# Kernel optimization log

Measured on AMD Instinct MI355X. Metric: run time of the kernel, lower is better.

The kernel has to match this reference:

```python
import jax, jax.numpy as jnp
import numpy as np

D_MODEL, D_INNER, D_STATE, D_CONV, NHEADS, HEADDIM, CHUNK = 2048, 4096, 128, 4, 64, 64, 64
CONV_DIM = D_INNER + 2 * D_STATE  # 4352
D_IN_PROJ = 2 * D_INNER + 2 * D_STATE + NHEADS  # 8512
EPS = 1e-5

def setup_inputs() -> dict:
    key = jax.random.key(0)
    ks = jax.random.split(key, 8)
    B, L = 2, 4096
    return {
        'u': jax.random.normal(ks[0], (B, L, D_MODEL), jnp.float32),
        'W_in': jax.random.normal(ks[1], (D_IN_PROJ, D_MODEL), jnp.float32) * 0.02,
        'conv_w': jax.random.normal(ks[2], (CONV_DIM, D_CONV), jnp.float32) * 0.2,
        'conv_b': jax.random.normal(ks[3], (CONV_DIM,), jnp.float32) * 0.02,
        'dt_bias': jax.random.normal(ks[4], (NHEADS,), jnp.float32) * 0.5,
        'A_log': jax.random.normal(ks[5], (NHEADS,), jnp.float32) * 0.5,
        'D': jax.random.normal(ks[6], (NHEADS,), jnp.float32),
        'norm_w': jnp.ones((D_INNER,), jnp.float32),
        'W_out': jax.random.normal(ks[7], (D_MODEL, D_INNER), jnp.float32) * 0.02,
    }

def silu(x):
    return x * jax.nn.sigmoid(x)

def segsum(x):
    # x: (..., T) -> (..., T, T); out[..., i, j] = sum_{j < k <= i} x[..., k], -inf above diag
    T = x.shape[-1]
    xr = jnp.broadcast_to(x[..., None], x.shape + (T,))
    m1 = jnp.tril(jnp.ones((T, T), bool), -1)
    s = jnp.cumsum(jnp.where(m1, xr, 0.0), axis=-2)
    m0 = jnp.tril(jnp.ones((T, T), bool), 0)
    return jnp.where(m0, s, -jnp.inf)

def ssd(x, A, B, C, chunk):
    # x: (b,L,h,p)  A: (b,L,h)  B,C: (b,L,n) shared across heads
    b, L, h, p = x.shape
    c = L // chunk
    x = x.reshape(b, c, chunk, h, p)
    A = A.reshape(b, c, chunk, h).transpose(0, 3, 1, 2)  # b h c l
    B = B.reshape(b, c, chunk, -1)
    C = C.reshape(b, c, chunk, -1)
    A_cs = jnp.cumsum(A, axis=-1)
    Lmat = jnp.exp(segsum(A))  # (b,h,c,l,s)
    Y_diag = jnp.einsum('bcln,bcsn,bhcls,bcshp->bclhp', C, B, Lmat, x)
    decay_states = jnp.exp(A_cs[..., -1:] - A_cs)  # (b,h,c,l)
    states = jnp.einsum('bcln,bhcl,bclhp->bchpn', B, decay_states, x)
    states = jnp.concatenate([jnp.zeros_like(states[:, :1]), states], axis=1)
    A_last = jnp.pad(A_cs[..., -1], ((0, 0), (0, 0), (1, 0)))  # (b,h,c+1)
    decay_chunk = jnp.exp(segsum(A_last))  # (b,h,c+1,c+1)
    new_states = jnp.einsum('bhzc,bchpn->bzhpn', decay_chunk, states)
    states, final = new_states[:, :-1], new_states[:, -1]
    sdo = jnp.exp(A_cs)  # (b,h,c,l)
    Y_off = jnp.einsum('bcln,bchpn,bhcl->bclhp', C, states, sdo)
    return (Y_diag + Y_off).reshape(b, L, h, p), final

def reference(u, W_in, conv_w, conv_b, dt_bias, A_log, D, norm_w, W_out):
    b, L, _ = u.shape
    zxbcdt = jnp.einsum('bld,ed->ble', u, W_in)
    z = zxbcdt[..., :D_INNER]
    xBC = zxbcdt[..., D_INNER:D_INNER + CONV_DIM]
    dt = jax.nn.softplus(zxbcdt[..., -NHEADS:] + dt_bias)  # (b,L,h)
    A = -jnp.exp(A_log)
    da_log = dt * A  # (b,L,h)
    # causal depthwise conv1d (kernel D_CONV, left pad D_CONV-1)
    xp = jnp.pad(xBC, ((0, 0), (D_CONV - 1, 0), (0, 0)))
    xBC = sum(xp[:, k:k + L, :] * conv_w[:, k] for k in range(D_CONV)) + conv_b
    xBC = silu(xBC)
    x = xBC[..., :D_INNER].reshape(b, L, NHEADS, HEADDIM)
    Bm = xBC[..., D_INNER:D_INNER + D_STATE]
    Cm = xBC[..., D_INNER + D_STATE:]
    y, final_state = ssd(x * dt[..., None], da_log, Bm, Cm, CHUNK)
    y = y + x * D[None, None, :, None]
    y = y.reshape(b, L, D_INNER)
    y = y * silu(z)
    y = y * jax.lax.rsqrt(jnp.mean(y * y, axis=-1, keepdims=True) + EPS) * norm_w
    return jnp.einsum('bld,ed->ble', y, W_out)
```

## Files before the change

### kernel.cpp

```cpp
#include <hip/hip_runtime.h>
#include <stdint.h>
#include <stddef.h>

#define SEQ     4096
#define DMODEL  2048
#define DINNER  4096
#define DSTATE  128
#define NH      64
#define HD      64
#define NCHUNK  64
#define CONVDIM 4352
#define DPROJ   8512

typedef __bf16 bf16_t;
typedef __bf16 bf16x8 __attribute__((ext_vector_type(8)));
typedef float  f32x4  __attribute__((ext_vector_type(4)));
typedef unsigned short u16x4 __attribute__((ext_vector_type(4)));

__device__ __forceinline__ void async_cp16(const bf16_t* g, bf16_t* l) {
    __builtin_amdgcn_global_load_lds(
        (const __attribute__((address_space(1))) void*)g,
        (__attribute__((address_space(3))) void*)l,
        16, 0, 0);
}

__global__ __launch_bounds__(256) void zero_out_kernel(float* out, int n) {
    int i = blockIdx.x*256 + threadIdx.x;
    if (i < n) out[i] = 0.f;
}

__global__ void detect_kernel(const unsigned short* norm_w_raw, int* flag) {
    if (threadIdx.x == 0 && blockIdx.x == 0)
        *flag = (norm_w_raw[0] == 0x3F80) ? 1 : 0;
}

__global__ __launch_bounds__(256) void cast_kernel(
    const void* __restrict__ src, size_t elem_off, bf16_t* __restrict__ dst,
    int n, const int* __restrict__ flag)
{
    int i = blockIdx.x*256 + threadIdx.x;
    if (i >= n) return;
    if (*flag) dst[i] = ((const bf16_t*)src)[elem_off + i];
    else       dst[i] = (bf16_t)(((const float*)src)[elem_off + i]);
}

__global__ __launch_bounds__(256) void cast4_kernel(
    const void* __restrict__ src, size_t elem_off, bf16_t* __restrict__ dst,
    int n4, const int* __restrict__ flag)
{
    int i = blockIdx.x*256 + threadIdx.x;
    if (i >= n4) return;
    if (*flag) {
        u16x4 v = *(const u16x4*)((const unsigned short*)src + elem_off + (size_t)i*4);
        *(u16x4*)(dst + (size_t)i*4) = v;
    } else {
        f32x4 v = *(const f32x4*)((const float*)src + elem_off + (size_t)i*4);
        bf16_t o[4];
        #pragma unroll
        for (int j = 0; j < 4; j++) o[j] = (bf16_t)v[j];
        *(u16x4*)(dst + (size_t)i*4) = *(const u16x4*)o;
    }
}

__global__ __launch_bounds__(256) void addp_kernel(
    float* __restrict__ out, const float* __restrict__ part, int n4)
{
    int i = blockIdx.x*256 + threadIdx.x;
    if (i >= n4) return;
    f32x4 a = *(const f32x4*)(out + (size_t)i*4);
    f32x4 b = *(const f32x4*)(part + (size_t)i*4);
    a[0]+=b[0]; a[1]+=b[1]; a[2]+=b[2]; a[3]+=b[3];
    *(f32x4*)(out + (size_t)i*4) = a;
}

__device__ __forceinline__ void stage_half(
    const bf16_t* __restrict__ G, int grow0, int gmaxrow, int gld,
    int kt, bf16_t* lplane, int half, int tid)
{
    #pragma unroll
    for (int q = 0; q < 2; q++) {
        int rloc = half*128 + q*64 + (tid >> 3);
        int grow = grow0 + rloc; if (grow > gmaxrow) grow = gmaxrow;
        int gcol = kt + ((((tid & 7) ^ (rloc & 7))) << 3);
        async_cp16(G + (size_t)grow*gld + gcol, lplane + rloc*64 + ((tid & 7) << 3));
    }
}

#define GMM_READ_A(PLANE, KS)                                                  \
    _Pragma("unroll")                                                          \
    for (int m_ = 0; m_ < 8; m_++) {                                           \
        const int rl_ = wmBase + m_*16 + lrow;                                 \
        afr[m_] = *(const bf16x8*)((PLANE) + rl_*64 + ((((KS)*4+quad) ^ (rl_&7))<<3)); \
    }

#define GMM_READ_B(PLANE, KS, DST)                                             \
    _Pragma("unroll")                                                          \
    for (int n_ = 0; n_ < 4; n_++) {                                           \
        const int rl_ = wnBase + n_*16 + lrow;                                 \
        DST[n_] = *(const bf16x8*)((PLANE) + rl_*64 + ((((KS)*4+quad) ^ (rl_&7))<<3)); \
    }

#define GMM_TAIL(BKARR, NA, NB)                                                \
    __builtin_amdgcn_s_barrier();                                              \
    asm volatile("s_waitcnt lgkmcnt(0)" ::: "memory");                         \
    __builtin_amdgcn_sched_barrier(0);                                         \
    __builtin_amdgcn_s_setprio(1);                                             \
    _Pragma("unroll")                                                          \
    for (int m_ = 0; m_ < 8; m_++) {                                           \
        acc[m_][NA] = __builtin_amdgcn_mfma_f32_16x16x32_bf16(afr[m_], BKARR[NA], acc[m_][NA], 0,0,0); \
        acc[m_][NB] = __builtin_amdgcn_mfma_f32_16x16x32_bf16(afr[m_], BKARR[NB], acc[m_][NB], 0,0,0); \
    }                                                                          \
    __builtin_amdgcn_s_setprio(0);

template <typename OT>
__global__ __launch_bounds__(512, 2) void gemm256_kernel(
    const bf16_t* __restrict__ A, const bf16_t* __restrict__ W,
    OT* C, OT* C2, int M, int N, int K, int lda, int khalf2)
{
    extern __shared__ __align__(16) bf16_t lds[];
    bf16_t* lAa = lds;
    bf16_t* lAb = lds + 16384;
    bf16_t* lBa = lds + 32768;
    bf16_t* lBb = lds + 49152;

    const int tid  = threadIdx.x;
    const int lane = tid & 63;
    const int wid  = tid >> 6;
    const int lrow = lane & 15;
    const int quad = lane >> 4;
    const int wmBase = (wid >> 2) * 128;
    const int wnBase = (wid & 3) * 64;

    int wg = blockIdx.x;
    const int nwg = gridDim.x;
    if ((nwg & 7) == 0) { int cpx = nwg >> 3; wg = (wg & 7)*cpx + (wg >> 3); }

    const int wld = K;
    int kloc = K;
    OT* Cw = C;
    if (khalf2) {
        const int htiles = nwg >> 1;
        kloc = K >> 1;
        if (wg >= htiles) { Cw = C2; wg -= htiles; A += kloc; W += kloc; }
    }

    const int ntx = (N + 255) >> 8;
    const int n0 = (wg % ntx) * 256;
    const int m0 = (wg / ntx) * 256;

    const int NT   = kloc >> 6;
    const int NTm1 = NT - 1;
    const int NT2  = NT >> 1;

    f32x4 acc[8][4] = {};
    bf16x8 afr[8], bk0[4], bk1[4];

    stage_half(A, m0, M-1, lda, 0,  lAa, 0, tid);
    stage_half(A, m0, M-1, lda, 0,  lAa, 1, tid);
    stage_half(W, n0, N-1, wld, 0,  lBa, 0, tid);
    stage_half(W, n0, N-1, wld, 0,  lBa, 1, tid);
    stage_half(A, m0, M-1, lda, 64, lAb, 0, tid);
    asm volatile("s_waitcnt vmcnt(2)" ::: "memory");
    __builtin_amdgcn_s_barrier();

    for (int i = 0; i < NT2; i++) {
        const int ktb = (2*i + 1) * 64;
        const int ktc = ((2*i + 2) & NTm1) * 64;
        const int ktd = ((2*i + 3) & NTm1) * 64;

        GMM_READ_A(lAa, 0)
        GMM_READ_B(lBa, 0, bk0)
        stage_half(A, m0, M-1, lda, ktb, lAb, 1, tid);
        asm volatile("s_waitcnt lgkmcnt(8)" ::: "memory");
        GMM_TAIL(bk0, 0, 1)
        __builtin_amdgcn_s_barrier();
        GMM_READ_B(lBa, 1, bk1)
        stage_half(W, n0, N-1, wld, ktb, lBb, 0, tid);
        GMM_TAIL(bk0, 2, 3)
        __builtin_amdgcn_s_barrier();
        GMM_READ_A(lAa, 1)
        stage_half(W, n0, N-1, wld, ktb, lBb, 1, tid);
        GMM_TAIL(bk1, 0, 1)
        __builtin_amdgcn_s_barrier();
        stage_half(A, m0, M-1, lda, ktc, lAa, 0, tid);
        GMM_TAIL(bk1, 2, 3)
        asm volatile("s_waitcnt vmcnt(2)" ::: "memory");
        __builtin_amdgcn_s_barrier();

        GMM_READ_A(lAb, 0)
        GMM_READ_B(lBb, 0, bk0)
        stage_half(A, m0, M-1, lda, ktc, lAa, 1, tid);
        asm volatile("s_waitcnt lgkmcnt(8)" ::: "memory");
        GMM_TAIL(bk0, 0, 1)
        __builtin_amdgcn_s_barrier();
        GMM_READ_B(lBb, 1, bk1)
        stage_half(W, n0, N-1, wld, ktc, lBa, 0, tid);
        GMM_TAIL(bk0, 2, 3)
        __builtin_amdgcn_s_barrier();
        GMM_READ_A(lAb, 1)
        stage_half(W, n0, N-1, wld, ktc, lBa, 1, tid);
        GMM_TAIL(bk1, 0, 1)
        __builtin_amdgcn_s_barrier();
        stage_half(A, m0, M-1, lda, ktd, lAb, 0, tid);
        GMM_TAIL(bk1, 2, 3)
        asm volatile("s_waitcnt vmcnt(2)" ::: "memory");
        __builtin_amdgcn_s_barrier();
    }

    asm volatile("s_waitcnt vmcnt(0)" ::: "memory");

    #pragma unroll
    for (int m = 0; m < 8; m++) {
        const int row = m0 + wmBase + m*16 + quad*4;
        #pragma unroll
        for (int n = 0; n < 4; n++) {
            const int col = n0 + wnBase + n*16 + lrow;
            if (col < N) {
                #pragma unroll
                for (int rr = 0; rr < 4; rr++)
                    Cw[(size_t)(row + rr)*N + col] = (OT)acc[m][n][rr];
            }
        }
    }
}

__global__ __launch_bounds__(256) void dt_kernel(
    const bf16_t* __restrict__ zx, const bf16_t* __restrict__ dt_bias,
    float* __restrict__ dtb)
{
    int i = blockIdx.x*256 + threadIdx.x;
    int h = i & 63, row = i >> 6;
    float raw = (float)zx[(size_t)row*DPROJ + (DINNER + CONVDIM) + h] + (float)dt_bias[h];
    dtb[i] = (raw > 20.f) ? raw : log1pf(expf(raw));
}

__global__ void cumsum_kernel(
    const float* __restrict__ dtb, const bf16_t* __restrict__ A_log,
    float* __restrict__ Acs)
{
    int blk = blockIdx.x;
    int h = blk & 63, c = blk >> 6;
    int lane = threadIdx.x;
    float Ah = -expf((float)A_log[h]);
    size_t row = (size_t)c*64 + lane;
    float v = dtb[row*64 + h] * Ah;
    #pragma unroll
    for (int off = 1; off < 64; off <<= 1) {
        float t = __shfl_up(v, off, 64);
        if (lane >= off) v += t;
    }
    Acs[(size_t)blk*64 + lane] = v;
}

__global__ __launch_bounds__(256) void conv_kernel(
    const bf16_t* __restrict__ zx, const bf16_t* __restrict__ conv_w,
    const bf16_t* __restrict__ conv_b, bf16_t* __restrict__ xbc)
{
    int i = blockIdx.x*256 + threadIdx.x;
    int cb = i % (CONVDIM/8);
    int l  = i / (CONVDIM/8);
    int ch0 = cb*8;
    const bf16_t* src = zx + (size_t)l*DPROJ + DINNER + ch0;
    float acc[8];
    {
        bf16x8 bv = *(const bf16x8*)(conv_b + ch0);
        #pragma unroll
        for (int j = 0; j < 8; j++) acc[j] = (float)bv[j];
    }
    bf16x8 w4[4];
    #pragma unroll
    for (int t = 0; t < 4; t++) w4[t] = *(const bf16x8*)(conv_w + ch0*4 + t*8);
    #pragma unroll
    for (int k = 0; k < 4; k++) {
        int ll = l - 3 + k;
        if (ll >= 0) {
            bf16x8 v = *(const bf16x8*)(src + (ptrdiff_t)(k-3)*DPROJ);
            #pragma unroll
            for (int j = 0; j < 8; j++)
                acc[j] += (float)v[j] * (float)w4[(j*4+k)>>3][(j*4+k)&7];
        }
    }
    bf16x8 o;
    #pragma unroll
    for (int j = 0; j < 8; j++)
        o[j] = (bf16_t)(acc[j] / (1.f + expf(-acc[j])));
    *(bf16x8*)(xbc + (size_t)i*8) = o;
}

__global__ __launch_bounds__(256) void states_kernel(
    const bf16_t* __restrict__ xbc, const float* __restrict__ dtb,
    const float* __restrict__ Acs, bf16_t* __restrict__ states)
{
    __shared__ __align__(16) bf16_t XsT[64*64];
    __shared__ __align__(16) bf16_t BT[128*64];
    __shared__ float AcsS[64];
    __shared__ float scaleS[64];
    const int blk = blockIdx.x;
    const int h = blk & 63, c = blk >> 6;
    const int tid = threadIdx.x, lane = tid & 63, wid = tid >> 6;
    const size_t rowbase = (size_t)c*64;

    if (tid < 64) AcsS[tid] = Acs[(size_t)blk*64 + tid];
    __syncthreads();
    if (tid < 64) scaleS[tid] = dtb[(rowbase + tid)*64 + h] * expf(AcsS[63] - AcsS[tid]);
    __syncthreads();

    {
        bf16x8 xa[2], b0[2], b1[2];
        #pragma unroll
        for (int half = 0; half < 2; half++) {
            #pragma unroll
            for (int j = 0; j < 8; j++) {
                int l = wid*16 + half*8 + j;
                const bf16_t* rp = xbc + (rowbase + l)*CONVDIM;
                xa[half][j] = (bf16_t)((float)rp[h*64 + lane] * scaleS[l]);
                b0[half][j] = rp[DINNER + lane];
                b1[half][j] = rp[DINNER + 64 + lane];
            }
        }
        #pragma unroll
        for (int half = 0; half < 2; half++) {
            int cch = wid*2 + half;
            *(bf16x8*)(XsT + lane*64       + ((cch ^ (lane & 7))*8)) = xa[half];
            *(bf16x8*)(BT  + lane*64       + ((cch ^ (lane & 7))*8)) = b0[half];
            *(bf16x8*)(BT  + (lane+64)*64  + ((cch ^ (lane & 7))*8)) = b1[half];
        }
    }
    __syncthreads();

    const int lrow = lane & 15, quad = lane >> 4;
    const int waveM = (wid & 1) * 32;
    const int waveN = (wid >> 1) * 64;
    f32x4 acc[2][4] = {};
    #pragma unroll
    for (int ks = 0; ks < 2; ks++) {
        bf16x8 af[2], bfr[4];
        #pragma unroll
        for (int i = 0; i < 2; i++) {
            int p = waveM + i*16 + lrow;
            af[i] = *(const bf16x8*)(XsT + p*64 + (((ks*4 + quad) ^ (p & 7))*8));
        }
        #pragma unroll
        for (int j = 0; j < 4; j++) {
            int n = waveN + j*16 + lrow;
            bfr[j] = *(const bf16x8*)(BT + n*64 + (((ks*4 + quad) ^ (n & 7))*8));
        }
        #pragma unroll
        for (int i = 0; i < 2; i++)
            #pragma unroll
            for (int j = 0; j < 4; j++)
                acc[i][j] = __builtin_amdgcn_mfma_f32_16x16x32_bf16(af[i], bfr[j], acc[i][j], 0, 0, 0);
    }

    const size_t sbase = (size_t)blk*8192;
    #pragma unroll
    for (int i = 0; i < 2; i++)
        #pragma unroll
        for (int j = 0; j < 4; j++) {
            int n = waveN + j*16 + lrow;
            #pragma unroll
            for (int r = 0; r < 4; r++) {
                int p = waveM + i*16 + quad*4 + r;
                states[sbase + (size_t)p*128 + n] = (bf16_t)acc[i][j][r];
            }
        }
}

__global__ __launch_bounds__(256) void gmat_kernel(
    const bf16_t* __restrict__ xbc, float* __restrict__ Gt)
{
    __shared__ __align__(16) float Ct[128*64];
    __shared__ __align__(16) float Bs2[64*128];
    int c = blockIdx.x;
    int tid = threadIdx.x;
    size_t rowbase = (size_t)c*64;
    for (int e = tid; e < 8192; e += 256) {
        int l = e >> 7, n = e & 127;
        const bf16_t* rp = xbc + (rowbase + l)*CONVDIM + DINNER;
        Bs2[e] = (float)rp[n];
        Ct[n*64 + (l ^ (n & 63))] = (float)rp[128 + n];
    }
    __syncthreads();
    int l = tid & 63, s0 = (tid >> 6) * 16;
    float acc[16] = {};
    for (int n4 = 0; n4 < 128; n4 += 4) {
        float c0 = Ct[(n4+0)*64 + (l ^ ((n4+0) & 63))];
        float c1 = Ct[(n4+1)*64 + (l ^ ((n4+1) & 63))];
        float c2 = Ct[(n4+2)*64 + (l ^ ((n4+2) & 63))];
        float c3 = Ct[(n4+3)*64 + (l ^ ((n4+3) & 63))];
        #pragma unroll
        for (int j = 0; j < 16; j++) {
            f32x4 bv = *(const f32x4*)&Bs2[(s0+j)*128 + n4];
            acc[j] += c0*bv[0] + c1*bv[1] + c2*bv[2] + c3*bv[3];
        }
    }
    float* gp = Gt + (size_t)c*4096;
    #pragma unroll
    for (int j = 0; j < 16; j++) gp[l*64 + (s0+j)] = acc[j];
}

__global__ __launch_bounds__(256) void scan_kernel(
    bf16_t* __restrict__ states, const float* __restrict__ Acs)
{
    int i = blockIdx.x*256 + threadIdx.x;
    int n = i & 127, p = (i >> 7) & 63, h = i >> 13;
    size_t off = (size_t)h*8192 + (size_t)p*128 + n;
    const float* ac = Acs + (size_t)h*64 + 63;
    float S = 0.f;
    for (int c = 0; c < 64; c++) {
        float tmp = (float)states[off];
        states[off] = (bf16_t)S;
        S = expf(ac[(size_t)c*4096]) * S + tmp;
        off += (size_t)64*8192;
    }
}

__global__ __launch_bounds__(256) void y_kernel(
    const bf16_t* __restrict__ xbc, const float* __restrict__ dtb,
    const float* __restrict__ Acs, const float* __restrict__ Gt,
    const bf16_t* __restrict__ states, const bf16_t* __restrict__ Dvec,
    bf16_t* __restrict__ y)
{
    __shared__ __align__(16) bf16_t Cs[64*128];
    __shared__ __align__(16) bf16_t Ss[64*128];
    __shared__ __align__(16) bf16_t Wm[64*64];
    __shared__ __align__(16) bf16_t XdT[64*64];
    __shared__ float acsS[64];
    __shared__ float dtS[64];
    const int blk = blockIdx.x;
    const int h = blk & 63, c = blk >> 6;
    const int tid = threadIdx.x, lane = tid & 63, wid = tid >> 6;
    const size_t rowbase = (size_t)c*64;
    const size_t sbase = (size_t)blk*8192;

    if (tid < 64) {
        acsS[tid] = Acs[(size_t)blk*64 + tid];
        dtS[tid]  = dtb[(rowbase + tid)*64 + h];
    }
    __syncthreads();

    #pragma unroll
    for (int it = 0; it < 4; it++) {
        int q = wid*256 + it*64 + lane;
        int l = q >> 4;
        int cl = (q & 15) ^ (l & 7);
        async_cp16(xbc + (rowbase + l)*CONVDIM + DINNER + 128 + cl*8,
                   Cs + (size_t)(wid*256 + it*64)*8);
        async_cp16(states + sbase + (size_t)l*128 + cl*8,
                   Ss + (size_t)(wid*256 + it*64)*8);
    }

    {
        const float* gp = Gt + (size_t)c*4096;
        #pragma unroll
        for (int k = 0; k < 16; k++) {
            int e = k*256 + tid;
            int l = e >> 6, s = e & 63;
            float w = 0.f;
            if (s <= l) w = gp[e] * expf(acsS[l] - acsS[s]);
            Wm[l*64 + (((s >> 3) ^ (l & 7))*8) + (s & 7)] = (bf16_t)w;
        }
    }

    {
        bf16x8 xd[2];
        #pragma unroll
        for (int half = 0; half < 2; half++)
            #pragma unroll
            for (int j = 0; j < 8; j++) {
                int s = wid*16 + half*8 + j;
                xd[half][j] = (bf16_t)((float)xbc[(rowbase + s)*CONVDIM + h*64 + lane] * dtS[s]);
            }
        #pragma unroll
        for (int half = 0; half < 2; half++) {
            int cch = wid*2 + half;
            *(bf16x8*)(XdT + lane*64 + ((cch ^ (lane & 7))*8)) = xd[half];
        }
    }
    __syncthreads();

    const int lrow = lane & 15, quad = lane >> 4;
    const int waveM = (wid & 1) * 32;
    const int waveN = (wid >> 1) * 32;
    f32x4 acc[2][2] = {};

    #pragma unroll
    for (int ks = 0; ks < 4; ks++) {
        bf16x8 af[2], bfr[2];
        #pragma unroll
        for (int i = 0; i < 2; i++) {
            int l = waveM + i*16 + lrow;
            af[i] = *(const bf16x8*)(Cs + l*128 + (((ks*4 + quad) ^ (l & 7))*8));
        }
        #pragma unroll
        for (int j = 0; j < 2; j++) {
            int p = waveN + j*16 + lrow;
            bfr[j] = *(const bf16x8*)(Ss + p*128 + (((ks*4 + quad) ^ (p & 7))*8));
        }
        #pragma unroll
        for (int i = 0; i < 2; i++)
            #pragma unroll
            for (int j = 0; j < 2; j++)
                acc[i][j] = __builtin_amdgcn_mfma_f32_16x16x32_bf16(af[i], bfr[j], acc[i][j], 0, 0, 0);
    }

    #pragma unroll
    for (int i = 0; i < 2; i++)
        #pragma unroll
        for (int r = 0; r < 4; r++) {
            int l = waveM + i*16 + quad*4 + r;
            float el = expf(acsS[l]);
            #pragma unroll
            for (int j = 0; j < 2; j++)
                acc[i][j][r] *= el;
        }

    #pragma unroll
    for (int ks = 0; ks < 2; ks++) {
        bf16x8 af[2], bfr[2];
        #pragma unroll
        for (int i = 0; i < 2; i++) {
            int l = waveM + i*16 + lrow;
            af[i] = *(const bf16x8*)(Wm + l*64 + (((ks*4 + quad) ^ (l & 7))*8));
        }
        #pragma unroll
        for (int j = 0; j < 2; j++) {
            int p = waveN + j*16 + lrow;
            bfr[j] = *(const bf16x8*)(XdT + p*64 + (((ks*4 + quad) ^ (p & 7))*8));
        }
        #pragma unroll
        for (int i = 0; i < 2; i++)
            #pragma unroll
            for (int j = 0; j < 2; j++)
                acc[i][j] = __builtin_amdgcn_mfma_f32_16x16x32_bf16(af[i], bfr[j], acc[i][j], 0, 0, 0);
    }

    const float Dh = (float)Dvec[h];
    #pragma unroll
    for (int i = 0; i < 2; i++)
        #pragma unroll
        for (int r = 0; r < 4; r++) {
            int l = waveM + i*16 + quad*4 + r;
            const bf16_t* xr = xbc + (rowbase + l)*CONVDIM + h*64;
            bf16_t* yr = y + (rowbase + l)*DPROJ + h*64;
            #pragma unroll
            for (int j = 0; j < 2; j++) {
                int p = waveN + j*16 + lrow;
                yr[p] = (bf16_t)(acc[i][j][r] + Dh * (float)xr[p]);
            }
        }
}

__global__ __launch_bounds__(256) void gatenorm_kernel(
    bf16_t* __restrict__ zx, const bf16_t* __restrict__ norm_w)
{
    __shared__ float red[4];
    int row = blockIdx.x;
    int tid = threadIdx.x;
    const bf16_t* zr = zx + (size_t)row*DPROJ;
    bf16_t* yr = zx + (size_t)row*DPROJ + DINNER;
    float vals[16]; float ss = 0.f;
    #pragma unroll
    for (int i = 0; i < 16; i++) {
        int e = i*256 + tid;
        float zv = (float)zr[e];
        float g = (float)yr[e] * (zv / (1.f + expf(-zv)));
        vals[i] = g; ss += g*g;
    }
    #pragma unroll
    for (int off = 32; off >= 1; off >>= 1) ss += __shfl_down(ss, off, 64);
    if ((tid & 63) == 0) red[tid >> 6] = ss;
    __syncthreads();
    float tot = red[0] + red[1] + red[2] + red[3];
    float scale = rsqrtf(tot * (1.f/4096.f) + 1e-5f);
    #pragma unroll
    for (int i = 0; i < 16; i++) {
        int e = i*256 + tid;
        yr[e] = (bf16_t)(vals[i] * scale * (float)norm_w[e]);
    }
}

extern "C" void kernel_launch(void* const* d_in, const int* in_sizes, int n_in,
                              void* d_out, int out_size, void* d_ws, size_t ws_size,
                              hipStream_t stream)
{
    const void* u_raw      = d_in[0];
    const void* W_in_raw   = d_in[1];
    const void* conv_w_raw = d_in[2];
    const void* conv_b_raw = d_in[3];
    const void* dt_b_raw   = d_in[4];
    const void* A_log_raw  = d_in[5];
    const void* D_raw      = d_in[6];
    const void* norm_w_raw = d_in[7];
    const void* W_out_raw  = d_in[8];
    float* out = (float*)d_out;

    const size_t SZ_HDR = 256 + 65536;
    const size_t SZ_ZX  = (size_t)SEQ*DPROJ*2;
    const size_t SZ_XBC = (size_t)SEQ*CONVDIM*2;
    const size_t SZ_ST  = (size_t)4096*8192*2;
    const size_t SZ_DTB = (size_t)SEQ*64*4;
    const size_t SZ_ACS = (size_t)4096*64*4;
    const size_t SZ_GT  = (size_t)64*4096*4;
    const size_t REQ = SZ_HDR + SZ_ZX + SZ_XBC + SZ_ST + SZ_DTB + SZ_ACS + SZ_GT;

    if (ws_size < REQ) {
        zero_out_kernel<<<(out_size + 255)/256, 256, 0, stream>>>(out, out_size);
        return;
    }

    static int smem_set = 0;
    if (!smem_set) {
        hipFuncSetAttribute(reinterpret_cast<const void*>(gemm256_kernel<bf16_t>),
                            hipFuncAttributeMaxDynamicSharedMemorySize, 131072);
        hipFuncSetAttribute(reinterpret_cast<const void*>(gemm256_kernel<float>),
                            hipFuncAttributeMaxDynamicSharedMemorySize, 131072);
        smem_set = 1;
    }

    char* w = (char*)d_ws;
    int*    flag   = (int*)w;            w += 256;
    bf16_t* smallb = (bf16_t*)w;         w += 65536;
    bf16_t* zx     = (bf16_t*)w;         w += SZ_ZX;
    bf16_t* xbc    = (bf16_t*)w;         w += SZ_XBC;
    bf16_t* states = (bf16_t*)w;         w += SZ_ST;
    float*  dtb    = (float*)w;          w += SZ_DTB;
    float*  Acs    = (float*)w;          w += SZ_ACS;
    float*  Gt     = (float*)w;          w += SZ_GT;
    bf16_t* yb     = zx + DINNER;
    float*  gpart  = (float*)xbc;

    bf16_t* conv_w_b  = smallb;
    bf16_t* conv_b_b  = smallb + 17408;
    bf16_t* dt_bias_b = smallb + 21760;
    bf16_t* A_log_b   = smallb + 21824;
    bf16_t* D_b       = smallb + 21888;
    bf16_t* norm_w_b  = smallb + 21952;
    bf16_t* u_b    = states;
    bf16_t* W_in_b = states + (size_t)SEQ*DMODEL;
    bf16_t* W_out_b = states;

    dim3 blk(256);
    detect_kernel<<<1, 1, 0, stream>>>((const unsigned short*)norm_w_raw, flag);
    cast_kernel<<<(17408+255)/256, blk, 0, stream>>>(conv_w_raw, 0, conv_w_b, 17408, flag);
    cast_kernel<<<(4352+255)/256,  blk, 0, stream>>>(conv_b_raw, 0, conv_b_b, 4352, flag);
    cast_kernel<<<1,               blk, 0, stream>>>(dt_b_raw,   0, dt_bias_b, 64, flag);
    cast_kernel<<<1,               blk, 0, stream>>>(A_log_raw,  0, A_log_b, 64, flag);
    cast_kernel<<<1,               blk, 0, stream>>>(D_raw,      0, D_b, 64, flag);
    cast_kernel<<<16,              blk, 0, stream>>>(norm_w_raw, 0, norm_w_b, 4096, flag);

    for (int b = 0; b < 2; b++) {
        float* outb = out + (size_t)b*SEQ*DMODEL;
        cast4_kernel<<<8192,  blk, 0, stream>>>(u_raw, (size_t)b*SEQ*DMODEL, u_b, SEQ*DMODEL/4, flag);
        cast4_kernel<<<17024, blk, 0, stream>>>(W_in_raw, 0, W_in_b, DPROJ*DMODEL/4, flag);
        gemm256_kernel<bf16_t><<<dim3(34*16), dim3(512), 131072, stream>>>(
            u_b, W_in_b, zx, zx, SEQ, DPROJ, DMODEL, DMODEL, 0);
        dt_kernel<<<1024, blk, 0, stream>>>(zx, dt_bias_b, dtb);
        cumsum_kernel<<<4096, 64, 0, stream>>>(dtb, A_log_b, Acs);
        conv_kernel<<<8704, blk, 0, stream>>>(zx, conv_w_b, conv_b_b, xbc);
        states_kernel<<<4096, blk, 0, stream>>>(xbc, dtb, Acs, states);
        gmat_kernel<<<64, blk, 0, stream>>>(xbc, Gt);
        scan_kernel<<<2048, blk, 0, stream>>>(states, Acs);
        y_kernel<<<4096, blk, 0, stream>>>(xbc, dtb, Acs, Gt, states, D_b, yb);
        cast4_kernel<<<8192, blk, 0, stream>>>(W_out_raw, 0, W_out_b, DMODEL*DINNER/4, flag);
        gatenorm_kernel<<<4096, blk, 0, stream>>>(zx, norm_w_b);
        gemm256_kernel<float><<<dim3(2*8*16), dim3(512), 131072, stream>>>(
            yb, W_out_b, outb, gpart, SEQ, DMODEL, DINNER, DPROJ, 1);
        addp_kernel<<<8192, blk, 0, stream>>>(outb, gpart, SEQ*DMODEL/4);
    }
}
```

Before: 1.053 ms.

## Split in-projection GEMM into full tiles plus split-K tail for ragged columns

```diff
diff --git a/kernel.cpp b/kernel.cpp
--- a/kernel.cpp
+++ b/kernel.cpp
@@ -71,6 +71,18 @@
     f32x4 b = *(const f32x4*)(part + (size_t)i*4);
     a[0]+=b[0]; a[1]+=b[1]; a[2]+=b[2]; a[3]+=b[3];
     *(f32x4*)(out + (size_t)i*4) = a;
+}
+
+#define TAILN 320
+#define TAILSZ (4096*TAILN)
+__global__ __launch_bounds__(256) void addp_tail_kernel(
+    bf16_t* __restrict__ zx_, const float* __restrict__ part)
+{
+    int i = blockIdx.x*256 + threadIdx.x;
+    if (i >= TAILSZ) return;
+    int r = i / TAILN, c = i - r*TAILN;
+    float v = part[i] + part[i + TAILSZ] + part[i + 2*TAILSZ] + part[i + 3*TAILSZ];
+    zx_[(size_t)r*DPROJ + 8192 + c] = (bf16_t)v;
 }
 
 __device__ __forceinline__ void stage_half(
@@ -115,7 +127,8 @@
 template <typename OT>
 __global__ __launch_bounds__(512, 2) void gemm256_kernel(
     const bf16_t* __restrict__ A, const bf16_t* __restrict__ W,
-    OT* C, OT* C2, int M, int N, int K, int lda, int khalf2)
+    OT* C, OT* Cpart, int M, int N, int K, int lda, int ldc,
+    int ksplit, int partall, int psz)
 {
     extern __shared__ __align__(16) bf16_t lds[];
     bf16_t* lAa = lds;
@@ -138,10 +151,13 @@
     const int wld = K;
     int kloc = K;
     OT* Cw = C;
-    if (khalf2) {
-        const int htiles = nwg >> 1;
-        kloc = K >> 1;
-        if (wg >= htiles) { Cw = C2; wg -= htiles; A += kloc; W += kloc; }
+    if (ksplit > 1) {
+        const int tps = nwg / ksplit;
+        kloc = K / ksplit;
+        int s = wg / tps; wg -= s*tps;
+        A += (size_t)s*kloc; W += (size_t)s*kloc;
+        if (partall)      Cw = Cpart + (size_t)s*psz;
+        else if (s > 0)   Cw = Cpart + (size_t)(s-1)*psz;
     }
 
     const int ntx = (N + 255) >> 8;
@@ -218,7 +234,7 @@
             if (col < N) {
                 #pragma unroll
                 for (int rr = 0; rr < 4; rr++)
-                    Cw[(size_t)(row + rr)*N + col] = (OT)acc[m][n][rr];
+                    Cw[(size_t)(row + rr)*ldc + col] = (OT)acc[m][n][rr];
             }
         }
     }
@@ -653,8 +669,12 @@
         float* outb = out + (size_t)b*SEQ*DMODEL;
         cast4_kernel<<<8192,  blk, 0, stream>>>(u_raw, (size_t)b*SEQ*DMODEL, u_b, SEQ*DMODEL/4, flag);
         cast4_kernel<<<17024, blk, 0, stream>>>(W_in_raw, 0, W_in_b, DPROJ*DMODEL/4, flag);
-        gemm256_kernel<bf16_t><<<dim3(34*16), dim3(512), 131072, stream>>>(
-            u_b, W_in_b, zx, zx, SEQ, DPROJ, DMODEL, DMODEL, 0);
+        gemm256_kernel<bf16_t><<<dim3(512), dim3(512), 131072, stream>>>(
+            u_b, W_in_b, zx, zx, SEQ, 8192, DMODEL, DMODEL, DPROJ, 1, 0, 0);
+        gemm256_kernel<float><<<dim3(128), dim3(512), 131072, stream>>>(
+            u_b, W_in_b + (size_t)8192*DMODEL, gpart, gpart,
+            SEQ, TAILN, DMODEL, DMODEL, TAILN, 4, 1, TAILSZ);
+        addp_tail_kernel<<<(TAILSZ+255)/256, blk, 0, stream>>>(zx, gpart);
         dt_kernel<<<1024, blk, 0, stream>>>(zx, dt_bias_b, dtb);
         cumsum_kernel<<<4096, 64, 0, stream>>>(dtb, A_log_b, Acs);
         conv_kernel<<<8704, blk, 0, stream>>>(zx, conv_w_b, conv_b_b, xbc);
@@ -664,8 +684,8 @@
         y_kernel<<<4096, blk, 0, stream>>>(xbc, dtb, Acs, Gt, states, D_b, yb);
         cast4_kernel<<<8192, blk, 0, stream>>>(W_out_raw, 0, W_out_b, DMODEL*DINNER/4, flag);
         gatenorm_kernel<<<4096, blk, 0, stream>>>(zx, norm_w_b);
-        gemm256_kernel<float><<<dim3(2*8*16), dim3(512), 131072, stream>>>(
-            yb, W_out_b, outb, gpart, SEQ, DMODEL, DINNER, DPROJ, 1);
+        gemm256_kernel<float><<<dim3(256), dim3(512), 131072, stream>>>(
+            yb, W_out_b, outb, gpart, SEQ, DMODEL, DINNER, DPROJ, DMODEL, 2, 0, SEQ*DMODEL);
         addp_kernel<<<8192, blk, 0, stream>>>(outb, gpart, SEQ*DMODEL/4);
     }
 }
```

Measured after the change: 1.012 ms. 1.04x faster.
